# Performance work log

Hardware: AMD Instinct MI355X
Metric: run time of the kernel (lower is better)

The kernel has to match this reference:

```python
import jax, jax.numpy as jnp
import numpy as np

NUM_EMBEDDINGS = 1024
EMBEDDING_DIM = 64
COMMITMENT_COST = 0.25
EPSILON = 1e-10


def setup_inputs() -> dict:
    key = jax.random.key(0)
    k1, k2 = jax.random.split(key)
    z_e = jax.random.normal(k1, (32, EMBEDDING_DIM, 64, 64), dtype=jnp.float32)
    # torch init: uniform(-1/K, 1/K)
    lim = 1.0 / NUM_EMBEDDINGS
    embedding = jax.random.uniform(k2, (NUM_EMBEDDINGS, EMBEDDING_DIM),
                                   dtype=jnp.float32, minval=-lim, maxval=lim)
    return {"z_e": z_e, "embedding": embedding}


def reference(z_e, embedding):
    # NCHW -> NHWC
    z = jnp.transpose(z_e, (0, 2, 3, 1))  # [B,H,W,D]
    input_shape = z.shape
    flat = z.reshape(-1, EMBEDDING_DIM)  # [N,D]

    x2 = jnp.sum(flat ** 2, axis=1, keepdims=True)          # [N,1]
    e2 = jnp.sum(embedding ** 2, axis=1)                     # [K]
    ip = jnp.matmul(flat, embedding.T)                       # [N,K]
    distances = x2 + e2 - 2.0 * ip

    encoding_indices = jnp.argmin(distances, axis=1)         # [N]
    encodings = jax.nn.one_hot(encoding_indices, NUM_EMBEDDINGS,
                               dtype=jnp.float32)            # [N,K]

    z_q = jnp.matmul(encodings, embedding).reshape(input_shape)  # [B,H,W,D]

    commitment_loss = COMMITMENT_COST * jnp.mean((jax.lax.stop_gradient(z_q) - z) ** 2)
    e2z_loss = jnp.mean((z_q - jax.lax.stop_gradient(z)) ** 2)
    vq_loss = commitment_loss + e2z_loss

    # straight-through estimator
    z_q = z + jax.lax.stop_gradient(z_q - z)

    avg_probs = jnp.mean(encodings, axis=0)  # [K]
    perplexity = jnp.exp(-jnp.sum(avg_probs * jnp.log(avg_probs + EPSILON)))

    z_q_out = jnp.transpose(z_q, (0, 3, 1, 2))  # back to NCHW
    return (vq_loss, z_q_out, perplexity, encodings)
```

## Files before the change

kernel.cpp:

```cpp
#include <hip/hip_runtime.h>
#include <cfloat>
#include <stdint.h>


typedef __attribute__((ext_vector_type(8))) short bf8v;
typedef __attribute__((ext_vector_type(4))) float f4v;

__device__ __forceinline__ unsigned short f2bf(float v) {
  unsigned u = __float_as_uint(v);
  return (unsigned short)((u + 0x7FFFu + ((u >> 16) & 1u)) >> 16);
}
__device__ __forceinline__ float bf2f(unsigned short h) {
  return __uint_as_float(((unsigned)h) << 16);
}

__global__ __launch_bounds__(256) void vq_prep(const float* __restrict__ emb,
                                               float* __restrict__ ws) {
  #pragma clang fp contract(off)
  int gid = blockIdx.x * 256 + threadIdx.x;
  if (gid == 0) ws[0] = 0.0f;
  ((int*)ws)[1 + gid] = 0;
  const float* e = emb + (gid << 6);
  float r[8];
  #pragma unroll
  for (int j = 0; j < 8; ++j) r[j] = e[j] * e[j];
  #pragma unroll
  for (int i = 8; i < 64; i += 8) {
    #pragma unroll
    for (int j = 0; j < 8; ++j) { float s = e[i + j] * e[i + j]; r[j] = r[j] + s; }
  }
  ws[1025 + gid] = ((r[0] + r[1]) + (r[2] + r[3])) + ((r[4] + r[5]) + (r[6] + r[7]));
}

__global__ __launch_bounds__(256) void vq_prep_frags(const float* __restrict__ emb,
                                                     float* __restrict__ out) {
  int e = blockIdx.x * 256 + threadIdx.x;
  int lane = e & 63, sub = e >> 6;
  int term = sub % 3, kk = (sub / 3) & 1, nt = sub / 6;
  int code = nt * 16 + (lane & 15);
  int d0 = kk * 32 + (lane >> 4) * 8;
  const float* src = emb + code * 64 + d0;
  unsigned short hs[8];
  #pragma unroll
  for (int j = 0; j < 8; ++j) {
    float v = src[j];
    unsigned short h = f2bf(v);  float r1 = v - bf2f(h);
    unsigned short m = f2bf(r1); float r2 = r1 - bf2f(m);
    unsigned short l = f2bf(r2);
    hs[j] = (term == 0) ? h : (term == 1) ? m : l;
  }
  uint4 p;
  p.x = (unsigned)hs[0] | ((unsigned)hs[1] << 16);
  p.y = (unsigned)hs[2] | ((unsigned)hs[3] << 16);
  p.z = (unsigned)hs[4] | ((unsigned)hs[5] << 16);
  p.w = (unsigned)hs[6] | ((unsigned)hs[7] << 16);
  ((uint4*)(out + 4))[e] = p;
}

__global__ __launch_bounds__(256, 4) void vq_main(const float* __restrict__ ze,
                                                  const float* __restrict__ emb,
                                                  float* __restrict__ ws,
                                                  float* __restrict__ out) {
  __shared__ float xtile[64 * 68];
  __shared__ __align__(16) short bbuf[2 * 6 * 64 * 8];
  __shared__ float e2s[1024];
  __shared__ float x2s[64];
  __shared__ float sx[256];
  __shared__ int warr[64];
  __shared__ float red[4];

  int t = threadIdx.x;
  int w = __builtin_amdgcn_readfirstlane(t >> 6);
  int lane = t & 63;
  int g = blockIdx.x;
  int b = g >> 6, h = g & 63;
  int n0 = g << 6;

  const float* zebase = ze + ((size_t)b << 18) + (h << 6);
  #pragma unroll
  for (int i = 0; i < 16; ++i) {
    int d = w * 16 + i;
    xtile[lane * 68 + d] = zebase[d * 4096 + lane];
  }
  e2s[t] = ws[1025 + t];         e2s[256 + t] = ws[1281 + t];
  e2s[512 + t] = ws[1537 + t];   e2s[768 + t] = ws[1793 + t];
  __syncthreads();

  {
    #pragma clang fp contract(off)
    const float* xr = xtile + lane * 68;
    int j0 = 2 * w, j1 = 2 * w + 1;
    float v0 = xr[j0], v1 = xr[j1];
    float ra = v0 * v0, rb = v1 * v1;
    #pragma unroll
    for (int p = 1; p < 8; ++p) {
      float s0 = xr[8 * p + j0]; s0 = s0 * s0; ra = ra + s0;
      float s1 = xr[8 * p + j1]; s1 = s1 * s1; rb = rb + s1;
    }
    sx[lane * 4 + w] = ra + rb;
  }
  __syncthreads();
  if (t < 64) x2s[t] = (sx[t * 4] + sx[t * 4 + 1]) + (sx[t * 4 + 2] + sx[t * 4 + 3]);
  __syncthreads();

  int qd = lane >> 4, rr = lane & 15;
  const float* xr = xtile + (w * 16 + rr) * 68;
  bf8v Ah[2], Am[2], Al[2];
  #pragma unroll
  for (int kk = 0; kk < 2; ++kk) {
    #pragma unroll
    for (int j = 0; j < 8; ++j) {
      float v = xr[kk * 32 + qd * 8 + j];
      unsigned short hh = f2bf(v);  float r1 = v - bf2f(hh);
      unsigned short mm = f2bf(r1); float r2 = r1 - bf2f(mm);
      unsigned short ll = f2bf(r2);
      Ah[kk][j] = (short)hh; Am[kk][j] = (short)mm; Al[kk][j] = (short)ll;
    }
  }
  float x2v[4];
  #pragma unroll
  for (int r = 0; r < 4; ++r) x2v[r] = x2s[w * 16 + qd * 4 + r];

  const uint4* ft = (const uint4*)(out + 4);
  uint4* bput = (uint4*)bbuf;
  float* encbase = out + 8388610 + (size_t)n0 * 1024;
  const float2 z2 = make_float2(0.0f, 0.0f);

  for (int f = w; f < 6; f += 4) bput[f * 64 + lane] = ft[f * 64 + lane];
  __syncthreads();

  unsigned long long best[4] = {~0ULL, ~0ULL, ~0ULL, ~0ULL};

  #pragma unroll 1
  for (int nt = 0; nt < 64; ++nt) {
    int cur = nt & 1, nxt = cur ^ 1;
    uint4 pv0, pv1;
    if (nt < 63) {
      pv0 = ft[((nt + 1) * 6 + w) * 64 + lane];
      if (w < 2) pv1 = ft[((nt + 1) * 6 + w + 4) * 64 + lane];
    }
    float e2v = e2s[nt * 16 + (lane & 15)];
    f4v acc = {0.0f, 0.0f, 0.0f, 0.0f};
    const bf8v* bb = (const bf8v*)bbuf + cur * 6 * 64;
    #pragma unroll
    for (int kk = 0; kk < 2; ++kk) {
      bf8v Bh = bb[(kk * 3 + 0) * 64 + lane];
      bf8v Bm = bb[(kk * 3 + 1) * 64 + lane];
      bf8v Bl = bb[(kk * 3 + 2) * 64 + lane];
      acc = __builtin_amdgcn_mfma_f32_16x16x32_bf16(Ah[kk], Bh, acc, 0, 0, 0);
      acc = __builtin_amdgcn_mfma_f32_16x16x32_bf16(Ah[kk], Bm, acc, 0, 0, 0);
      acc = __builtin_amdgcn_mfma_f32_16x16x32_bf16(Am[kk], Bh, acc, 0, 0, 0);
      acc = __builtin_amdgcn_mfma_f32_16x16x32_bf16(Am[kk], Bm, acc, 0, 0, 0);
      acc = __builtin_amdgcn_mfma_f32_16x16x32_bf16(Ah[kk], Bl, acc, 0, 0, 0);
      acc = __builtin_amdgcn_mfma_f32_16x16x32_bf16(Al[kk], Bh, acc, 0, 0, 0);
    }
    unsigned code0 = (unsigned)(nt * 16 + (lane & 15));
    #pragma unroll
    for (int r = 0; r < 4; ++r) {
      float tt = x2v[r] + e2v;
      float dd = fmaf(-2.0f, acc[r], tt);
      unsigned long long cand =
          (((unsigned long long)__float_as_uint(dd)) << 32) | code0;
      if (cand < best[r]) best[r] = cand;
    }
    float2* ez = (float2*)(encbase + nt * 1024) + t;
    ez[0] = z2; ez[256] = z2;
    if (nt < 63) {
      bput[(nxt * 6 + w) * 64 + lane] = pv0;
      if (w < 2) bput[(nxt * 6 + w + 4) * 64 + lane] = pv1;
    }
    __syncthreads();
  }

  #pragma unroll
  for (int r = 0; r < 4; ++r) {
    unsigned long long bu = best[r];
    #pragma unroll
    for (int m = 1; m <= 8; m <<= 1) {
      unsigned long long o = __shfl_xor(bu, m, 64);
      if (o < bu) bu = o;
    }
    best[r] = bu;
  }

  if (b == 0) {
    if ((lane & 15) == 0) {
      #pragma unroll
      for (int r = 0; r < 4; ++r)
        ((int*)encbase)[w * 16 + qd * 4 + r] = (int)(best[r] & 0xFFFFFFFFu);
    }
    return;
  }

  if ((lane & 15) == 0) {
    #pragma unroll
    for (int r = 0; r < 4; ++r)
      warr[w * 16 + qd * 4 + r] = (int)(best[r] & 0xFFFFFFFFu);
  }
  __syncthreads();

  if (t < 64) {
    int gi = warr[t];
    encbase[(size_t)t * 1024 + gi] = 1.0f;
    atomicAdd((int*)ws + 1 + gi, 1);
  }

  {
    int row = t & 63;
    int gi = warr[row];
    const float* er = emb + (gi << 6);
    const float* xz = xtile + row * 68;
    float* qr = out + 1 + ((size_t)b << 18) + (h << 6) + row;
    float ls = 0.0f;
    #pragma unroll
    for (int i = 0; i < 16; ++i) {
      int d = (t >> 6) * 16 + i;
      float v = er[d];
      float df = v - xz[d];
      ls = fmaf(df, df, ls);
      qr[(size_t)d * 4096] = v;
    }
    #pragma unroll
    for (int off = 32; off > 0; off >>= 1) ls += __shfl_down(ls, off, 64);
    if ((t & 63) == 0) red[t >> 6] = ls;
    __syncthreads();
    if (t == 0) atomicAdd(ws, (red[0] + red[1]) + (red[2] + red[3]));
  }
}

__global__ __launch_bounds__(256) void vq_out(const float* __restrict__ ze,
                                              const float* __restrict__ emb,
                                              float* __restrict__ ws,
                                              float* __restrict__ out) {
  __shared__ float red[4];
  int g = blockIdx.x, t = threadIdx.x;
  int b = g >> 6, h = g & 63, n0 = g << 6;
  float* enc = out + 8388610;
  int* wp = (int*)(enc + (size_t)n0 * 1024);
  int row = t & 63;
  int gi = wp[row];
  __syncthreads();
  if (t < 64) ((float*)wp)[t] = 0.0f;
  __syncthreads();
  if (t < 64) enc[(size_t)(n0 + t) * 1024 + gi] = 1.0f;

  const float* er = emb + gi * 64;
  const float* zr = ze + ((size_t)b << 18) + (h << 6) + row;
  float* qr = out + 1 + ((size_t)b << 18) + (h << 6) + row;
  float ls = 0.0f;
  #pragma unroll
  for (int i = 0; i < 16; ++i) {
    int d = (t >> 6) * 16 + i;
    float v = er[d];
    float df = v - zr[(size_t)d * 4096];
    ls = fmaf(df, df, ls);
    qr[(size_t)d * 4096] = v;
  }
  #pragma unroll
  for (int off = 32; off > 0; off >>= 1) ls += __shfl_down(ls, off, 64);
  if ((t & 63) == 0) red[t >> 6] = ls;
  __syncthreads();
  if (t == 0) atomicAdd(ws, (red[0] + red[1]) + (red[2] + red[3]));
  if (t < 64) atomicAdd((int*)ws + 1 + gi, 1);
}

__global__ __launch_bounds__(1024) void vq_fin(const float* __restrict__ ws,
                                               float* __restrict__ out) {
  __shared__ float sm[16];
  int t = threadIdx.x;
  const int* counts = (const int*)ws + 1;
  float c = (float)counts[t];
  float p = c * (1.0f / 131072.0f);
  float s = p * logf(p + 1e-10f);
  #pragma unroll
  for (int off = 32; off > 0; off >>= 1) s += __shfl_down(s, off, 64);
  if ((t & 63) == 0) sm[t >> 6] = s;
  __syncthreads();
  if (t == 0) {
    float v = 0.0f;
    #pragma unroll
    for (int i = 0; i < 16; ++i) v += sm[i];
    out[8388609] = expf(-v);
    float m = ws[0] / 8388608.0f;
    out[0] = 0.25f * m + m;
  }
}

extern "C" void kernel_launch(void* const* d_in, const int* in_sizes, int n_in,
                              void* d_out, int out_size, void* d_ws, size_t ws_size,
                              hipStream_t stream) {
  const float* ze  = (const float*)d_in[0];
  const float* emb = (const float*)d_in[1];
  float* out = (float*)d_out;
  float* ws  = (float*)d_ws;
  vq_prep<<<4, 256, 0, stream>>>(emb, ws);
  vq_prep_frags<<<96, 256, 0, stream>>>(emb, out);
  vq_main<<<2048, 256, 0, stream>>>(ze, emb, ws, out);
  vq_out<<<64, 256, 0, stream>>>(ze, emb, ws, out);
  vq_fin<<<1, 1024, 0, stream>>>(ws, out);
}
```

Before: 641.5 us.

## Process two code tiles per iteration and alias x tile with B buffer

The distance loop now handles two 16-code tiles per iteration, with two independent MFMA accumulator chains, halving the barrier count and issuing wider 16-byte zero stores for the encodings. The x tile shared buffer is aliased with the double-buffered B staging area to cap LDS use, which requires an extra barrier and means the loss epilogue must re-read z_e from global memory instead of LDS. All threads now cooperatively load 768 uint4 per stage.

```diff
diff --git a/kernel.cpp b/kernel.cpp
--- a/kernel.cpp
+++ b/kernel.cpp
@@ -57,12 +57,28 @@
   ((uint4*)(out + 4))[e] = p;
 }
 
+#define TILE12(ACC, BH0, BM0, BL0, BH1, BM1, BL1) do {                         \
+    ACC = __builtin_amdgcn_mfma_f32_16x16x32_bf16(Ah[0], BH0, ACC, 0, 0, 0);   \
+    ACC = __builtin_amdgcn_mfma_f32_16x16x32_bf16(Ah[0], BM0, ACC, 0, 0, 0);   \
+    ACC = __builtin_amdgcn_mfma_f32_16x16x32_bf16(Am[0], BH0, ACC, 0, 0, 0);   \
+    ACC = __builtin_amdgcn_mfma_f32_16x16x32_bf16(Am[0], BM0, ACC, 0, 0, 0);   \
+    ACC = __builtin_amdgcn_mfma_f32_16x16x32_bf16(Ah[0], BL0, ACC, 0, 0, 0);   \
+    ACC = __builtin_amdgcn_mfma_f32_16x16x32_bf16(Al[0], BH0, ACC, 0, 0, 0);   \
+    ACC = __builtin_amdgcn_mfma_f32_16x16x32_bf16(Ah[1], BH1, ACC, 0, 0, 0);   \
+    ACC = __builtin_amdgcn_mfma_f32_16x16x32_bf16(Ah[1], BM1, ACC, 0, 0, 0);   \
+    ACC = __builtin_amdgcn_mfma_f32_16x16x32_bf16(Am[1], BH1, ACC, 0, 0, 0);   \
+    ACC = __builtin_amdgcn_mfma_f32_16x16x32_bf16(Am[1], BM1, ACC, 0, 0, 0);   \
+    ACC = __builtin_amdgcn_mfma_f32_16x16x32_bf16(Ah[1], BL1, ACC, 0, 0, 0);   \
+    ACC = __builtin_amdgcn_mfma_f32_16x16x32_bf16(Al[1], BH1, ACC, 0, 0, 0);   \
+  } while (0)
+
 __global__ __launch_bounds__(256, 4) void vq_main(const float* __restrict__ ze,
                                                   const float* __restrict__ emb,
                                                   float* __restrict__ ws,
                                                   float* __restrict__ out) {
-  __shared__ float xtile[64 * 68];
-  __shared__ __align__(16) short bbuf[2 * 6 * 64 * 8];
+  __shared__ __align__(16) unsigned char smem_u[2 * 768 * 16];
+  float* xtile = (float*)smem_u;
+  uint4* bput  = (uint4*)smem_u;
   __shared__ float e2s[1024];
   __shared__ float x2s[64];
   __shared__ float sx[256];
@@ -120,54 +136,58 @@
   float x2v[4];
   #pragma unroll
   for (int r = 0; r < 4; ++r) x2v[r] = x2s[w * 16 + qd * 4 + r];
+  __syncthreads();
 
   const uint4* ft = (const uint4*)(out + 4);
-  uint4* bput = (uint4*)bbuf;
   float* encbase = out + 8388610 + (size_t)n0 * 1024;
-  const float2 z2 = make_float2(0.0f, 0.0f);
-
-  for (int f = w; f < 6; f += 4) bput[f * 64 + lane] = ft[f * 64 + lane];
+  const f4v z4 = {0.0f, 0.0f, 0.0f, 0.0f};
+
+  bput[t] = ft[t]; bput[t + 256] = ft[t + 256]; bput[t + 512] = ft[t + 512];
   __syncthreads();
 
   unsigned long long best[4] = {~0ULL, ~0ULL, ~0ULL, ~0ULL};
 
   #pragma unroll 1
-  for (int nt = 0; nt < 64; ++nt) {
-    int cur = nt & 1, nxt = cur ^ 1;
-    uint4 pv0, pv1;
-    if (nt < 63) {
-      pv0 = ft[((nt + 1) * 6 + w) * 64 + lane];
-      if (w < 2) pv1 = ft[((nt + 1) * 6 + w + 4) * 64 + lane];
-    }
-    float e2v = e2s[nt * 16 + (lane & 15)];
-    f4v acc = {0.0f, 0.0f, 0.0f, 0.0f};
-    const bf8v* bb = (const bf8v*)bbuf + cur * 6 * 64;
-    #pragma unroll
-    for (int kk = 0; kk < 2; ++kk) {
-      bf8v Bh = bb[(kk * 3 + 0) * 64 + lane];
-      bf8v Bm = bb[(kk * 3 + 1) * 64 + lane];
-      bf8v Bl = bb[(kk * 3 + 2) * 64 + lane];
-      acc = __builtin_amdgcn_mfma_f32_16x16x32_bf16(Ah[kk], Bh, acc, 0, 0, 0);
-      acc = __builtin_amdgcn_mfma_f32_16x16x32_bf16(Ah[kk], Bm, acc, 0, 0, 0);
-      acc = __builtin_amdgcn_mfma_f32_16x16x32_bf16(Am[kk], Bh, acc, 0, 0, 0);
-      acc = __builtin_amdgcn_mfma_f32_16x16x32_bf16(Am[kk], Bm, acc, 0, 0, 0);
-      acc = __builtin_amdgcn_mfma_f32_16x16x32_bf16(Ah[kk], Bl, acc, 0, 0, 0);
-      acc = __builtin_amdgcn_mfma_f32_16x16x32_bf16(Al[kk], Bh, acc, 0, 0, 0);
-    }
-    unsigned code0 = (unsigned)(nt * 16 + (lane & 15));
+  for (int ii = 0; ii < 32; ++ii) {
+    int cur = ii & 1, nxt = cur ^ 1;
+    int nt0 = 2 * ii, nt1 = 2 * ii + 1;
+    uint4 pA, pB, pC;
+    if (ii < 31) {
+      int base = (ii + 1) * 768;
+      pA = ft[base + t]; pB = ft[base + t + 256]; pC = ft[base + t + 512];
+    }
+    float e2v0 = e2s[nt0 * 16 + (lane & 15)];
+    float e2v1 = e2s[nt1 * 16 + (lane & 15)];
+    f4v acc0 = {0.0f, 0.0f, 0.0f, 0.0f};
+    f4v acc1 = {0.0f, 0.0f, 0.0f, 0.0f};
+    const bf8v* bb = (const bf8v*)bput + cur * 768;
+    bf8v B0h0 = bb[0 * 64 + lane],  B0m0 = bb[1 * 64 + lane],  B0l0 = bb[2 * 64 + lane];
+    bf8v B0h1 = bb[3 * 64 + lane],  B0m1 = bb[4 * 64 + lane],  B0l1 = bb[5 * 64 + lane];
+    bf8v B1h0 = bb[6 * 64 + lane],  B1m0 = bb[7 * 64 + lane],  B1l0 = bb[8 * 64 + lane];
+    bf8v B1h1 = bb[9 * 64 + lane],  B1m1 = bb[10 * 64 + lane], B1l1 = bb[11 * 64 + lane];
+    TILE12(acc0, B0h0, B0m0, B0l0, B0h1, B0m1, B0l1);
+    TILE12(acc1, B1h0, B1m0, B1l0, B1h1, B1m1, B1l1);
+    unsigned code0 = (unsigned)(nt0 * 16 + (lane & 15));
+    unsigned code1 = (unsigned)(nt1 * 16 + (lane & 15));
     #pragma unroll
     for (int r = 0; r < 4; ++r) {
-      float tt = x2v[r] + e2v;
-      float dd = fmaf(-2.0f, acc[r], tt);
-      unsigned long long cand =
-          (((unsigned long long)__float_as_uint(dd)) << 32) | code0;
-      if (cand < best[r]) best[r] = cand;
-    }
-    float2* ez = (float2*)(encbase + nt * 1024) + t;
-    ez[0] = z2; ez[256] = z2;
-    if (nt < 63) {
-      bput[(nxt * 6 + w) * 64 + lane] = pv0;
-      if (w < 2) bput[(nxt * 6 + w + 4) * 64 + lane] = pv1;
+      float t0 = x2v[r] + e2v0;
+      float d0 = fmaf(-2.0f, acc0[r], t0);
+      unsigned long long c0 =
+          (((unsigned long long)__float_as_uint(d0)) << 32) | code0;
+      if (c0 < best[r]) best[r] = c0;
+      float t1 = x2v[r] + e2v1;
+      float d1 = fmaf(-2.0f, acc1[r], t1);
+      unsigned long long c1 =
+          (((unsigned long long)__float_as_uint(d1)) << 32) | code1;
+      if (c1 < best[r]) best[r] = c1;
+    }
+    f4v* ez = (f4v*)(encbase + nt0 * 1024) + t;
+    ez[0] = z4; ez[256] = z4;
+    if (ii < 31) {
+      bput[nxt * 768 + t] = pA;
+      bput[nxt * 768 + t + 256] = pB;
+      bput[nxt * 768 + t + 512] = pC;
     }
     __syncthreads();
   }
@@ -209,14 +229,14 @@
     int row = t & 63;
     int gi = warr[row];
     const float* er = emb + (gi << 6);
-    const float* xz = xtile + row * 68;
+    const float* zr = ze + ((size_t)b << 18) + (h << 6) + row;
     float* qr = out + 1 + ((size_t)b << 18) + (h << 6) + row;
     float ls = 0.0f;
     #pragma unroll
     for (int i = 0; i < 16; ++i) {
       int d = (t >> 6) * 16 + i;
       float v = er[d];
-      float df = v - xz[d];
+      float df = v - zr[(size_t)d * 4096];
       ls = fmaf(df, df, ls);
       qr[(size_t)d * 4096] = v;
     }
```

Result: no change. 641.9 us (+0.1%).

## Process two row tiles per block to share codebook fragments

Applied to the files above, without the earlier changes.

Each vq_main block now handles two 64-row tiles instead of one, halving the grid. Both tiles reuse the same LDS-staged codebook fragments and interleave two independent MFMA accumulation chains. Shared memory is overlaid in one union buffer, the x tile stride is narrowed, and the encoding zero-fill uses 16-byte stores. The loss pass now re-reads z from global memory because the x tiles are overwritten. In exchange, register pressure rises (six A fragment sets) and fewer blocks are available to hide latency.

```diff
diff --git a/kernel.cpp b/kernel.cpp
--- a/kernel.cpp
+++ b/kernel.cpp
@@ -61,26 +61,34 @@
                                                   const float* __restrict__ emb,
                                                   float* __restrict__ ws,
                                                   float* __restrict__ out) {
-  __shared__ float xtile[64 * 68];
-  __shared__ __align__(16) short bbuf[2 * 6 * 64 * 8];
+  __shared__ __align__(16) unsigned char U[36352];
+  float* xtA  = (float*)U;
+  float* xtB  = (float*)(U + 16896);
+  float* sx   = (float*)(U + 33792);
+  float* x2s  = (float*)(U + 35840);
+  uint4* bput = (uint4*)U;
+  int*   warr = (int*)(U + 12288);
+  float* red  = (float*)(U + 12800);
   __shared__ float e2s[1024];
-  __shared__ float x2s[64];
-  __shared__ float sx[256];
-  __shared__ int warr[64];
-  __shared__ float red[4];
 
   int t = threadIdx.x;
   int w = __builtin_amdgcn_readfirstlane(t >> 6);
   int lane = t & 63;
   int g = blockIdx.x;
-  int b = g >> 6, h = g & 63;
-  int n0 = g << 6;
-
-  const float* zebase = ze + ((size_t)b << 18) + (h << 6);
+  int gA = 2 * g, gB = 2 * g + 1;
+  int bA = gA >> 6, hA = gA & 63;
+  int bB = gB >> 6, hB = gB & 63;
+
+  float* encA = out + 8388610 + (size_t)gA * 65536;
+  float* encB = encA + 65536;
+
+  const float* zeA = ze + ((size_t)bA << 18) + (hA << 6);
+  const float* zeB = ze + ((size_t)bB << 18) + (hB << 6);
   #pragma unroll
   for (int i = 0; i < 16; ++i) {
     int d = w * 16 + i;
-    xtile[lane * 68 + d] = zebase[d * 4096 + lane];
+    xtA[lane * 66 + d] = zeA[(size_t)d * 4096 + lane];
+    xtB[lane * 66 + d] = zeB[(size_t)d * 4096 + lane];
   }
   e2s[t] = ws[1025 + t];         e2s[256 + t] = ws[1281 + t];
   e2s[512 + t] = ws[1537 + t];   e2s[768 + t] = ws[1793 + t];
@@ -88,48 +96,65 @@
 
   {
     #pragma clang fp contract(off)
-    const float* xr = xtile + lane * 68;
+    const float* xrA = xtA + lane * 66;
+    const float* xrB = xtB + lane * 66;
     int j0 = 2 * w, j1 = 2 * w + 1;
-    float v0 = xr[j0], v1 = xr[j1];
-    float ra = v0 * v0, rb = v1 * v1;
+    float vA0 = xrA[j0], vA1 = xrA[j1], vB0 = xrB[j0], vB1 = xrB[j1];
+    float ra = vA0 * vA0, rb = vA1 * vA1, rc = vB0 * vB0, rd = vB1 * vB1;
     #pragma unroll
     for (int p = 1; p < 8; ++p) {
-      float s0 = xr[8 * p + j0]; s0 = s0 * s0; ra = ra + s0;
-      float s1 = xr[8 * p + j1]; s1 = s1 * s1; rb = rb + s1;
+      float s0 = xrA[8 * p + j0]; s0 = s0 * s0; ra = ra + s0;
+      float s1 = xrA[8 * p + j1]; s1 = s1 * s1; rb = rb + s1;
+      float s2 = xrB[8 * p + j0]; s2 = s2 * s2; rc = rc + s2;
+      float s3 = xrB[8 * p + j1]; s3 = s3 * s3; rd = rd + s3;
     }
     sx[lane * 4 + w] = ra + rb;
-  }
-  __syncthreads();
-  if (t < 64) x2s[t] = (sx[t * 4] + sx[t * 4 + 1]) + (sx[t * 4 + 2] + sx[t * 4 + 3]);
+    sx[256 + lane * 4 + w] = rc + rd;
+  }
+  __syncthreads();
+  if (t < 64) {
+    x2s[t]      = (sx[t * 4] + sx[t * 4 + 1]) + (sx[t * 4 + 2] + sx[t * 4 + 3]);
+    x2s[64 + t] = (sx[256 + t * 4] + sx[256 + t * 4 + 1]) +
+                  (sx[256 + t * 4 + 2] + sx[256 + t * 4 + 3]);
+  }
   __syncthreads();
 
   int qd = lane >> 4, rr = lane & 15;
-  const float* xr = xtile + (w * 16 + rr) * 68;
-  bf8v Ah[2], Am[2], Al[2];
-  #pragma unroll
-  for (int kk = 0; kk < 2; ++kk) {
-    #pragma unroll
-    for (int j = 0; j < 8; ++j) {
-      float v = xr[kk * 32 + qd * 8 + j];
-      unsigned short hh = f2bf(v);  float r1 = v - bf2f(hh);
-      unsigned short mm = f2bf(r1); float r2 = r1 - bf2f(mm);
-      unsigned short ll = f2bf(r2);
-      Ah[kk][j] = (short)hh; Am[kk][j] = (short)mm; Al[kk][j] = (short)ll;
-    }
-  }
-  float x2v[4];
-  #pragma unroll
-  for (int r = 0; r < 4; ++r) x2v[r] = x2s[w * 16 + qd * 4 + r];
+  bf8v AhA[2], AmA[2], AlA[2], AhB[2], AmB[2], AlB[2];
+  {
+    const float* xrA = xtA + (w * 16 + rr) * 66;
+    const float* xrB = xtB + (w * 16 + rr) * 66;
+    #pragma unroll
+    for (int kk = 0; kk < 2; ++kk) {
+      #pragma unroll
+      for (int j = 0; j < 8; ++j) {
+        float v = xrA[kk * 32 + qd * 8 + j];
+        unsigned short hh = f2bf(v);  float r1 = v - bf2f(hh);
+        unsigned short mm = f2bf(r1); float r2 = r1 - bf2f(mm);
+        AhA[kk][j] = (short)hh; AmA[kk][j] = (short)mm; AlA[kk][j] = (short)f2bf(r2);
+        float u = xrB[kk * 32 + qd * 8 + j];
+        unsigned short h2 = f2bf(u);  float s1 = u - bf2f(h2);
+        unsigned short m2 = f2bf(s1); float s2 = s1 - bf2f(m2);
+        AhB[kk][j] = (short)h2; AmB[kk][j] = (short)m2; AlB[kk][j] = (short)f2bf(s2);
+      }
+    }
+  }
+  float x2vA[4], x2vB[4];
+  #pragma unroll
+  for (int r = 0; r < 4; ++r) {
+    x2vA[r] = x2s[w * 16 + qd * 4 + r];
+    x2vB[r] = x2s[64 + w * 16 + qd * 4 + r];
+  }
+  __syncthreads();
 
   const uint4* ft = (const uint4*)(out + 4);
-  uint4* bput = (uint4*)bbuf;
-  float* encbase = out + 8388610 + (size_t)n0 * 1024;
-  const float2 z2 = make_float2(0.0f, 0.0f);
+  const f4v z4 = {0.0f, 0.0f, 0.0f, 0.0f};
 
   for (int f = w; f < 6; f += 4) bput[f * 64 + lane] = ft[f * 64 + lane];
   __syncthreads();
 
-  unsigned long long best[4] = {~0ULL, ~0ULL, ~0ULL, ~0ULL};
+  unsigned long long bestA[4] = {~0ULL, ~0ULL, ~0ULL, ~0ULL};
+  unsigned long long bestB[4] = {~0ULL, ~0ULL, ~0ULL, ~0ULL};
 
   #pragma unroll 1
   for (int nt = 0; nt < 64; ++nt) {
@@ -140,31 +165,43 @@
       if (w < 2) pv1 = ft[((nt + 1) * 6 + w + 4) * 64 + lane];
     }
     float e2v = e2s[nt * 16 + (lane & 15)];
-    f4v acc = {0.0f, 0.0f, 0.0f, 0.0f};
-    const bf8v* bb = (const bf8v*)bbuf + cur * 6 * 64;
+    f4v accA = {0.0f, 0.0f, 0.0f, 0.0f};
+    f4v accB = {0.0f, 0.0f, 0.0f, 0.0f};
+    const bf8v* bb = (const bf8v*)bput + cur * 6 * 64;
     #pragma unroll
     for (int kk = 0; kk < 2; ++kk) {
       bf8v Bh = bb[(kk * 3 + 0) * 64 + lane];
       bf8v Bm = bb[(kk * 3 + 1) * 64 + lane];
       bf8v Bl = bb[(kk * 3 + 2) * 64 + lane];
-      acc = __builtin_amdgcn_mfma_f32_16x16x32_bf16(Ah[kk], Bh, acc, 0, 0, 0);
-      acc = __builtin_amdgcn_mfma_f32_16x16x32_bf16(Ah[kk], Bm, acc, 0, 0, 0);
-      acc = __builtin_amdgcn_mfma_f32_16x16x32_bf16(Am[kk], Bh, acc, 0, 0, 0);
-      acc = __builtin_amdgcn_mfma_f32_16x16x32_bf16(Am[kk], Bm, acc, 0, 0, 0);
-      acc = __builtin_amdgcn_mfma_f32_16x16x32_bf16(Ah[kk], Bl, acc, 0, 0, 0);
-      acc = __builtin_amdgcn_mfma_f32_16x16x32_bf16(Al[kk], Bh, acc, 0, 0, 0);
+      accA = __builtin_amdgcn_mfma_f32_16x16x32_bf16(AhA[kk], Bh, accA, 0, 0, 0);
+      accA = __builtin_amdgcn_mfma_f32_16x16x32_bf16(AhA[kk], Bm, accA, 0, 0, 0);
+      accA = __builtin_amdgcn_mfma_f32_16x16x32_bf16(AmA[kk], Bh, accA, 0, 0, 0);
+      accA = __builtin_amdgcn_mfma_f32_16x16x32_bf16(AmA[kk], Bm, accA, 0, 0, 0);
+      accA = __builtin_amdgcn_mfma_f32_16x16x32_bf16(AhA[kk], Bl, accA, 0, 0, 0);
+      accA = __builtin_amdgcn_mfma_f32_16x16x32_bf16(AlA[kk], Bh, accA, 0, 0, 0);
+      accB = __builtin_amdgcn_mfma_f32_16x16x32_bf16(AhB[kk], Bh, accB, 0, 0, 0);
+      accB = __builtin_amdgcn_mfma_f32_16x16x32_bf16(AhB[kk], Bm, accB, 0, 0, 0);
+      accB = __builtin_amdgcn_mfma_f32_16x16x32_bf16(AmB[kk], Bh, accB, 0, 0, 0);
+      accB = __builtin_amdgcn_mfma_f32_16x16x32_bf16(AmB[kk], Bm, accB, 0, 0, 0);
+      accB = __builtin_amdgcn_mfma_f32_16x16x32_bf16(AhB[kk], Bl, accB, 0, 0, 0);
+      accB = __builtin_amdgcn_mfma_f32_16x16x32_bf16(AlB[kk], Bh, accB, 0, 0, 0);
     }
     unsigned code0 = (unsigned)(nt * 16 + (lane & 15));
     #pragma unroll
     for (int r = 0; r < 4; ++r) {
-      float tt = x2v[r] + e2v;
-      float dd = fmaf(-2.0f, acc[r], tt);
-      unsigned long long cand =
-          (((unsigned long long)__float_as_uint(dd)) << 32) | code0;
-      if (cand < best[r]) best[r] = cand;
-    }
-    float2* ez = (float2*)(encbase + nt * 1024) + t;
-    ez[0] = z2; ez[256] = z2;
+      float tA = x2vA[r] + e2v;
+      float dA = fmaf(-2.0f, accA[r], tA);
+      unsigned long long cA =
+          (((unsigned long long)__float_as_uint(dA)) << 32) | code0;
+      if (cA < bestA[r]) bestA[r] = cA;
+      float tB = x2vB[r] + e2v;
+      float dB = fmaf(-2.0f, accB[r], tB);
+      unsigned long long cB =
+          (((unsigned long long)__float_as_uint(dB)) << 32) | code0;
+      if (cB < bestB[r]) bestB[r] = cB;
+    }
+    ((f4v*)(encA + nt * 1024))[t] = z4;
+    ((f4v*)(encB + nt * 1024))[t] = z4;
     if (nt < 63) {
       bput[(nxt * 6 + w) * 64 + lane] = pv0;
       if (w < 2) bput[(nxt * 6 + w + 4) * 64 + lane] = pv1;
@@ -174,57 +211,86 @@
 
   #pragma unroll
   for (int r = 0; r < 4; ++r) {
-    unsigned long long bu = best[r];
+    unsigned long long buA = bestA[r], buB = bestB[r];
     #pragma unroll
     for (int m = 1; m <= 8; m <<= 1) {
-      unsigned long long o = __shfl_xor(bu, m, 64);
-      if (o < bu) bu = o;
-    }
-    best[r] = bu;
-  }
-
-  if (b == 0) {
+      unsigned long long oA = __shfl_xor(buA, m, 64);
+      if (oA < buA) buA = oA;
+      unsigned long long oB = __shfl_xor(buB, m, 64);
+      if (oB < buB) buB = oB;
+    }
+    bestA[r] = buA; bestB[r] = buB;
+  }
+
+  if (bA == 0) {
     if ((lane & 15) == 0) {
       #pragma unroll
-      for (int r = 0; r < 4; ++r)
-        ((int*)encbase)[w * 16 + qd * 4 + r] = (int)(best[r] & 0xFFFFFFFFu);
+      for (int r = 0; r < 4; ++r) {
+        ((int*)encA)[w * 16 + qd * 4 + r] = (int)(bestA[r] & 0xFFFFFFFFu);
+        ((int*)encB)[w * 16 + qd * 4 + r] = (int)(bestB[r] & 0xFFFFFFFFu);
+      }
     }
     return;
   }
 
   if ((lane & 15) == 0) {
     #pragma unroll
-    for (int r = 0; r < 4; ++r)
-      warr[w * 16 + qd * 4 + r] = (int)(best[r] & 0xFFFFFFFFu);
-  }
-  __syncthreads();
-
-  if (t < 64) {
+    for (int r = 0; r < 4; ++r) {
+      warr[w * 16 + qd * 4 + r]      = (int)(bestA[r] & 0xFFFFFFFFu);
+      warr[64 + w * 16 + qd * 4 + r] = (int)(bestB[r] & 0xFFFFFFFFu);
+    }
+  }
+  __syncthreads();
+
+  if (t < 128) {
     int gi = warr[t];
-    encbase[(size_t)t * 1024 + gi] = 1.0f;
+    float* e = (t < 64) ? encA : encB;
+    e[(size_t)(t & 63) * 1024 + gi] = 1.0f;
     atomicAdd((int*)ws + 1 + gi, 1);
   }
 
   {
     int row = t & 63;
-    int gi = warr[row];
-    const float* er = emb + (gi << 6);
-    const float* xz = xtile + row * 68;
-    float* qr = out + 1 + ((size_t)b << 18) + (h << 6) + row;
-    float ls = 0.0f;
-    #pragma unroll
-    for (int i = 0; i < 16; ++i) {
-      int d = (t >> 6) * 16 + i;
-      float v = er[d];
-      float df = v - xz[d];
-      ls = fmaf(df, df, ls);
-      qr[(size_t)d * 4096] = v;
-    }
-    #pragma unroll
-    for (int off = 32; off > 0; off >>= 1) ls += __shfl_down(ls, off, 64);
-    if ((t & 63) == 0) red[t >> 6] = ls;
+    float lsA = 0.0f;
+    {
+      int gi = warr[row];
+      const float* er = emb + (gi << 6);
+      const float* zr = zeA + row;
+      float* qr = out + 1 + ((size_t)bA << 18) + (hA << 6) + row;
+      #pragma unroll
+      for (int i = 0; i < 16; ++i) {
+        int d = (t >> 6) * 16 + i;
+        float v = er[d];
+        float df = v - zr[(size_t)d * 4096];
+        lsA = fmaf(df, df, lsA);
+        qr[(size_t)d * 4096] = v;
+      }
+    }
+    float lsB = 0.0f;
+    {
+      int gi = warr[64 + row];
+      const float* er = emb + (gi << 6);
+      const float* zr = zeB + row;
+      float* qr = out + 1 + ((size_t)bB << 18) + (hB << 6) + row;
+      #pragma unroll
+      for (int i = 0; i < 16; ++i) {
+        int d = (t >> 6) * 16 + i;
+        float v = er[d];
+        float df = v - zr[(size_t)d * 4096];
+        lsB = fmaf(df, df, lsB);
+        qr[(size_t)d * 4096] = v;
+      }
+    }
+    #pragma unroll
+    for (int off = 32; off > 0; off >>= 1) {
+      lsA += __shfl_down(lsA, off, 64);
+      lsB += __shfl_down(lsB, off, 64);
+    }
+    if ((t & 63) == 0) { red[t >> 6] = lsA; red[4 + (t >> 6)] = lsB; }
     __syncthreads();
-    if (t == 0) atomicAdd(ws, (red[0] + red[1]) + (red[2] + red[3]));
+    if (t == 0)
+      atomicAdd(ws, ((red[0] + red[1]) + (red[2] + red[3])) +
+                    ((red[4] + red[5]) + (red[6] + red[7])));
   }
 }
 
@@ -295,7 +361,7 @@
   float* ws  = (float*)d_ws;
   vq_prep<<<4, 256, 0, stream>>>(emb, ws);
   vq_prep_frags<<<96, 256, 0, stream>>>(emb, out);
-  vq_main<<<2048, 256, 0, stream>>>(ze, emb, ws, out);
+  vq_main<<<1024, 256, 0, stream>>>(ze, emb, ws, out);
   vq_out<<<64, 256, 0, stream>>>(ze, emb, ws, out);
   vq_fin<<<1, 1024, 0, stream>>>(ws, out);
 }
```

After: 652.5 us. About the same (+1.7%).
